# Kernel tuning notes

Measured on AMD Instinct MI355X. Metric: run time of the kernel, lower is better.

The kernel has to match this reference:

```python
import jax, jax.numpy as jnp
import numpy as np

NEG_INF = -1.0e9  # value used by masked_fill in the original

def setup_inputs() -> dict:
    key = jax.random.key(0)
    kq, kk, kv, km = jax.random.split(key, 4)
    B, H, S, D = 2, 16, 2048, 64
    query = jax.random.normal(kq, (B, H, S, D), dtype=jnp.float32)
    key_t = jax.random.normal(kk, (B, H, S, D), dtype=jnp.float32)
    value = jax.random.normal(kv, (B, H, S, D), dtype=jnp.float32)
    mask = jax.random.randint(km, (1, 1, S, S), 0, 2, dtype=jnp.int32)
    return {"query": query, "key": key_t, "value": value, "mask": mask}

def reference(query, key, value, mask):
    d_k = query.shape[-1]
    # scores: [B,H,Sq,Sk]
    scores = jnp.einsum("bhqd,bhkd->bhqk", query, key) / jnp.sqrt(jnp.float32(d_k))
    scores = jnp.where(mask == 0, jnp.float32(NEG_INF), scores)
    attn = jax.nn.softmax(scores, axis=-1)
    out = jnp.einsum("bhqk,bhkd->bhqd", attn, value)
    return (out, attn)
```

## Files before the change

kernel.cpp:

```cpp
#include <hip/hip_runtime.h>


#define S_LEN 2048
#define D_DIM 64
#define BH_N  32
#define NELEM (BH_N*S_LEN*D_DIM)

typedef __bf16 bf16;
typedef bf16 bf16x4 __attribute__((ext_vector_type(4)));
typedef bf16 bf16x8 __attribute__((ext_vector_type(8)));
typedef float f32x4 __attribute__((ext_vector_type(4)));

__device__ __attribute__((aligned(16))) bf16 g_Qb[NELEM];
__device__ __attribute__((aligned(16))) bf16 g_Kb[NELEM];
__device__ __attribute__((aligned(16))) bf16 g_VT[NELEM];
__device__ unsigned long long g_bits[S_LEN*S_LEN/64];

__device__ __forceinline__ void gload16(const bf16* g, bf16* l){
  __builtin_amdgcn_global_load_lds(
      (const __attribute__((address_space(1))) void*)g,
      (__attribute__((address_space(3))) void*)l, 16, 0, 0);
}

__global__ void cvt_qk_kernel(const float* __restrict__ Qs, const float* __restrict__ Ks){
  int i = blockIdx.x*256 + threadIdx.x;
  float4 q = reinterpret_cast<const float4*>(Qs)[i];
  float4 k = reinterpret_cast<const float4*>(Ks)[i];
  bf16x4 oq = {(bf16)q.x,(bf16)q.y,(bf16)q.z,(bf16)q.w};
  bf16x4 ok = {(bf16)k.x,(bf16)k.y,(bf16)k.z,(bf16)k.w};
  ((bf16x4*)g_Qb)[i] = oq;
  ((bf16x4*)g_Kb)[i] = ok;
}

__global__ void transpose_v_kernel(const float* __restrict__ V){
  __shared__ float sv[64][65];
  int bh = blockIdx.x >> 5;
  int k0 = (blockIdx.x & 31) << 6;
  const float* src = V + ((size_t)bh*S_LEN + k0)*D_DIM;
  #pragma unroll
  for (int i=0;i<16;i++){
    int e = threadIdx.x + i*256;
    sv[e>>6][e&63] = src[e];
  }
  __syncthreads();
  bf16* dst = g_VT + (size_t)bh*D_DIM*S_LEN + k0;
  #pragma unroll
  for (int i=0;i<16;i++){
    int e = threadIdx.x + i*256;
    int d = e>>6, k = e&63;
    dst[(size_t)d*S_LEN + k] = (bf16)sv[k][d];
  }
}

__global__ void build_bits_kernel(const int* __restrict__ mask){
  int gid = blockIdx.x*256 + threadIdx.x;
  unsigned long long b = __ballot(mask[gid] != 0);
  if ((threadIdx.x & 63) == 0) g_bits[gid >> 6] = b;
}

__global__ __launch_bounds__(256, 4)
void attn_main_kernel(float* __restrict__ out, float* __restrict__ attn){
  __shared__ __attribute__((aligned(16))) bf16 s_pool[5*64*64];
  bf16* const kd0 = s_pool;
  bf16* const kd1 = s_pool + 4096;
  bf16* const vd0 = s_pool + 8192;
  bf16* const vd1 = s_pool + 12288;
  bf16* const sp  = s_pool + 16384;

  const int tid  = threadIdx.x;
  const int wave = tid >> 6, lane = tid & 63;
  const int quad = lane >> 4, l16 = lane & 15;

  const int logical = ((blockIdx.x & 7) << 7) | (blockIdx.x >> 3);
  const int bh = logical >> 5, qb = logical & 31;
  const int q0 = qb << 6, m0 = wave << 4;

  const bf16* __restrict__ Qh  = g_Qb + ((size_t)bh*S_LEN + q0)*D_DIM;
  const bf16* __restrict__ Kh  = g_Kb + (size_t)bh*S_LEN*D_DIM;
  const bf16* __restrict__ VTh = g_VT + (size_t)bh*D_DIM*S_LEN;
  float* __restrict__ outh  = out  + ((size_t)bh*S_LEN + q0)*D_DIM;
  float* __restrict__ attnh = attn + (size_t)bh*S_LEN*S_LEN + (size_t)q0*S_LEN;

  const int s0 = tid, s1 = tid + 256;
  const int r0 = s0>>3, b0 = (s0&7)^(r0&7);
  const int r1 = s1>>3, b1 = (s1&7)^(r1&7);
  const int    gk0 = r0*D_DIM + b0*8, gk1 = r1*D_DIM + b1*8;
  const size_t gv0 = (size_t)r0*S_LEN + b0*8, gv1 = (size_t)r1*S_LEN + b1*8;
  const int lb0 = (wave<<6)*8, lb1 = (256 + (wave<<6))*8;

  gload16(Qh  + gk0, sp  + lb0);  gload16(Qh  + gk1, sp  + lb1);
  gload16(Kh  + gk0, kd0 + lb0);  gload16(Kh  + gk1, kd0 + lb1);
  gload16(VTh + gv0, vd0 + lb0);  gload16(VTh + gv1, vd0 + lb1);
  __syncthreads();

  const int arow = m0 + l16;
  const bf16x8 aq0 = *(const bf16x8*)&sp[(arow<<6) + ((quad     ^ (arow&7))<<3)];
  const bf16x8 aq1 = *(const bf16x8*)&sp[(arow<<6) + (((quad+4) ^ (arow&7))<<3)];

  float lp[4] = {0.f,0.f,0.f,0.f};
  f32x4 oacc[4];
  #pragma unroll
  for (int n=0;n<4;n++) oacc[n] = (f32x4){0.f,0.f,0.f,0.f};

  const int mrow = q0 + m0 + quad*4;
  const size_t mbase = (size_t)mrow * 32;

  for (int kt=0; kt<32; ++kt){
    bf16* const kcur = (kt&1) ? kd1 : kd0;
    bf16* const vcur = (kt&1) ? vd1 : vd0;
    if (kt < 31){
      bf16* const knxt = (kt&1) ? kd0 : kd1;
      bf16* const vnxt = (kt&1) ? vd0 : vd1;
      const bf16* Ks = Kh  + (size_t)((kt+1)<<6)*D_DIM;
      const bf16* Vs = VTh + ((kt+1)<<6);
      gload16(Ks+gk0, knxt+lb0);  gload16(Ks+gk1, knxt+lb1);
      gload16(Vs+gv0, vnxt+lb0);  gload16(Vs+gv1, vnxt+lb1);
    }
    unsigned long long wr_[4];
    #pragma unroll
    for (int r=0;r<4;r++) wr_[r] = g_bits[mbase + r*32 + kt];

    #pragma unroll
    for (int n=0;n<4;n++){
      const int krow = n*16 + l16;
      const bf16x8 bk0 = *(const bf16x8*)&kcur[(krow<<6) + ((quad     ^ (krow&7))<<3)];
      const bf16x8 bk1 = *(const bf16x8*)&kcur[(krow<<6) + (((quad+4) ^ (krow&7))<<3)];
      __builtin_amdgcn_s_setprio(1);
      f32x4 c = (f32x4){0.f,0.f,0.f,0.f};
      c = __builtin_amdgcn_mfma_f32_16x16x32_bf16(aq0, bk0, c, 0,0,0);
      c = __builtin_amdgcn_mfma_f32_16x16x32_bf16(aq1, bk1, c, 0,0,0);
      __builtin_amdgcn_s_setprio(0);
      const int shift = n*16 + l16;
      #pragma unroll
      for (int r=0;r<4;r++){
        float p = ((wr_[r] >> shift) & 1ull) ? __expf(c[r]*0.125f) : 0.f;
        lp[r] += p;
        const int prow = m0 + quad*4 + r;
        sp[(prow<<6) + (((shift>>3)^(prow&7))<<3) + (shift&7)] = (bf16)p;
      }
    }

    __builtin_amdgcn_s_setprio(1);
    #pragma unroll
    for (int s=0;s<2;s++){
      const bf16x8 pa = *(const bf16x8*)&sp[(arow<<6) + (((s*4+quad)^(arow&7))<<3)];
      #pragma unroll
      for (int n=0;n<4;n++){
        const int vrow = n*16 + l16;
        const bf16x8 vb = *(const bf16x8*)&vcur[(vrow<<6) + (((s*4+quad)^(vrow&7))<<3)];
        oacc[n] = __builtin_amdgcn_mfma_f32_16x16x32_bf16(pa, vb, oacc[n], 0,0,0);
      }
    }
    __builtin_amdgcn_s_setprio(0);
    __syncthreads();
  }

  gload16(Kh+gk0, kd0+lb0);  gload16(Kh+gk1, kd0+lb1);

  #pragma unroll
  for (int r=0;r<4;r++){
    float v = lp[r];
    #pragma unroll
    for (int off=1; off<16; off<<=1) v += __shfl_xor(v, off);
    lp[r] = 1.0f / v;
  }

  #pragma unroll
  for (int n=0;n<4;n++){
    #pragma unroll
    for (int r=0;r<4;r++)
      outh[(size_t)(m0 + quad*4 + r)*D_DIM + n*16 + l16] = oacc[n][r] * lp[r];
  }

  __syncthreads();

  for (int kt=0; kt<32; ++kt){
    bf16* const kcur = (kt&1) ? kd1 : kd0;
    if (kt < 31){
      bf16* const knxt = (kt&1) ? kd0 : kd1;
      const bf16* Ks = Kh + (size_t)((kt+1)<<6)*D_DIM;
      gload16(Ks+gk0, knxt+lb0);  gload16(Ks+gk1, knxt+lb1);
    }
    unsigned long long wr_[4];
    #pragma unroll
    for (int r=0;r<4;r++) wr_[r] = g_bits[mbase + r*32 + kt];

    #pragma unroll
    for (int n=0;n<4;n++){
      const int krow = n*16 + l16;
      const bf16x8 bk0 = *(const bf16x8*)&kcur[(krow<<6) + ((quad     ^ (krow&7))<<3)];
      const bf16x8 bk1 = *(const bf16x8*)&kcur[(krow<<6) + (((quad+4) ^ (krow&7))<<3)];
      __builtin_amdgcn_s_setprio(1);
      f32x4 c = (f32x4){0.f,0.f,0.f,0.f};
      c = __builtin_amdgcn_mfma_f32_16x16x32_bf16(aq0, bk0, c, 0,0,0);
      c = __builtin_amdgcn_mfma_f32_16x16x32_bf16(aq1, bk1, c, 0,0,0);
      __builtin_amdgcn_s_setprio(0);
      const int shift = n*16 + l16;
      #pragma unroll
      for (int r=0;r<4;r++){
        float a = ((wr_[r] >> shift) & 1ull) ? __expf(c[r]*0.125f)*lp[r] : 0.f;
        attnh[(size_t)(m0 + quad*4 + r)*S_LEN + (kt<<6) + shift] = a;
      }
    }
    __syncthreads();
  }
}

extern "C" void kernel_launch(void* const* d_in, const int* in_sizes, int n_in,
                              void* d_out, int out_size, void* d_ws, size_t ws_size,
                              hipStream_t stream){
  (void)in_sizes; (void)n_in; (void)d_ws; (void)ws_size; (void)out_size;
  const float* Q    = (const float*)d_in[0];
  const float* K    = (const float*)d_in[1];
  const float* V    = (const float*)d_in[2];
  const int*   mask = (const int*)d_in[3];
  float* out  = (float*)d_out;
  float* attn = out + (size_t)NELEM;

  cvt_qk_kernel     <<<NELEM/4/256,        256, 0, stream>>>(Q, K);
  transpose_v_kernel<<<BH_N*(S_LEN/64),    256, 0, stream>>>(V);
  build_bits_kernel <<<S_LEN*S_LEN/256,    256, 0, stream>>>(mask);
  attn_main_kernel  <<<BH_N*(S_LEN/64),    256, 0, stream>>>(out, attn);
}
```

Measured before the change: 700.0 us.

## Split key tile across wave pairs with 512-thread blocks and LDS reduction

Doubles the block to 8 waves. Each pair of waves shares a 16-row query slice and splits the 64-key tile in half, covering both the QK^T/softmax step and the PV accumulation. The partial row sums and output accumulators are combined through LDS before normalisation. The aim is more waves in flight to hide memory latency on the bandwidth-bound attention write. The cost is extra LDS traffic, an added barrier, and register pressure from the tighter launch bounds.

New measurement: 1.053 ms. 1.5x slower.

```diff
diff --git a/kernel.cpp b/kernel.cpp
--- a/kernel.cpp
+++ b/kernel.cpp
@@ -58,22 +58,26 @@
   if ((threadIdx.x & 63) == 0) g_bits[gid >> 6] = b;
 }
 
-__global__ __launch_bounds__(256, 4)
+__global__ __launch_bounds__(512, 8)
 void attn_main_kernel(float* __restrict__ out, float* __restrict__ attn){
-  __shared__ __attribute__((aligned(16))) bf16 s_pool[5*64*64];
+  __shared__ __attribute__((aligned(16))) bf16 s_pool[5*4096];
   bf16* const kd0 = s_pool;
   bf16* const kd1 = s_pool + 4096;
   bf16* const vd0 = s_pool + 8192;
   bf16* const vd1 = s_pool + 12288;
   bf16* const sp  = s_pool + 16384;
+  float* const obuf = (float*)(s_pool + 8192);
+  float* const lsum = (float*)(s_pool + 16384);
 
   const int tid  = threadIdx.x;
   const int wave = tid >> 6, lane = tid & 63;
   const int quad = lane >> 4, l16 = lane & 15;
+  const int mh = wave >> 1, kh = wave & 1;
+  const int m0 = mh << 4;
 
   const int logical = ((blockIdx.x & 7) << 7) | (blockIdx.x >> 3);
   const int bh = logical >> 5, qb = logical & 31;
-  const int q0 = qb << 6, m0 = wave << 4;
+  const int q0 = qb << 6;
 
   const bf16* __restrict__ Qh  = g_Qb + ((size_t)bh*S_LEN + q0)*D_DIM;
   const bf16* __restrict__ Kh  = g_Kb + (size_t)bh*S_LEN*D_DIM;
@@ -81,21 +85,20 @@
   float* __restrict__ outh  = out  + ((size_t)bh*S_LEN + q0)*D_DIM;
   float* __restrict__ attnh = attn + (size_t)bh*S_LEN*S_LEN + (size_t)q0*S_LEN;
 
-  const int s0 = tid, s1 = tid + 256;
-  const int r0 = s0>>3, b0 = (s0&7)^(r0&7);
-  const int r1 = s1>>3, b1 = (s1&7)^(r1&7);
-  const int    gk0 = r0*D_DIM + b0*8, gk1 = r1*D_DIM + b1*8;
-  const size_t gv0 = (size_t)r0*S_LEN + b0*8, gv1 = (size_t)r1*S_LEN + b1*8;
-  const int lb0 = (wave<<6)*8, lb1 = (256 + (wave<<6))*8;
-
-  gload16(Qh  + gk0, sp  + lb0);  gload16(Qh  + gk1, sp  + lb1);
-  gload16(Kh  + gk0, kd0 + lb0);  gload16(Kh  + gk1, kd0 + lb1);
-  gload16(VTh + gv0, vd0 + lb0);  gload16(VTh + gv1, vd0 + lb1);
+  const int r0 = tid >> 3, b0 = (tid & 7) ^ (r0 & 7);
+  const int    gk = r0*D_DIM + b0*8;
+  const size_t gv = (size_t)r0*S_LEN + b0*8;
+  const int lb = wave << 9;
+
+  gload16(Qh + gk,  sp  + lb);
+  gload16(Kh + gk,  kd0 + lb);
+  gload16(VTh + gv, vd0 + lb);
   __syncthreads();
 
   const int arow = m0 + l16;
   const bf16x8 aq0 = *(const bf16x8*)&sp[(arow<<6) + ((quad     ^ (arow&7))<<3)];
   const bf16x8 aq1 = *(const bf16x8*)&sp[(arow<<6) + (((quad+4) ^ (arow&7))<<3)];
+  __syncthreads();
 
   float lp[4] = {0.f,0.f,0.f,0.f};
   f32x4 oacc[4];
@@ -111,17 +114,16 @@
     if (kt < 31){
       bf16* const knxt = (kt&1) ? kd0 : kd1;
       bf16* const vnxt = (kt&1) ? vd0 : vd1;
-      const bf16* Ks = Kh  + (size_t)((kt+1)<<6)*D_DIM;
-      const bf16* Vs = VTh + ((kt+1)<<6);
-      gload16(Ks+gk0, knxt+lb0);  gload16(Ks+gk1, knxt+lb1);
-      gload16(Vs+gv0, vnxt+lb0);  gload16(Vs+gv1, vnxt+lb1);
+      gload16(Kh  + (size_t)((kt+1)<<6)*D_DIM + gk, knxt + lb);
+      gload16(VTh + ((kt+1)<<6) + gv,               vnxt + lb);
     }
     unsigned long long wr_[4];
     #pragma unroll
     for (int r=0;r<4;r++) wr_[r] = g_bits[mbase + r*32 + kt];
 
     #pragma unroll
-    for (int n=0;n<4;n++){
+    for (int g=0; g<2; ++g){
+      const int n = kh*2 + g;
       const int krow = n*16 + l16;
       const bf16x8 bk0 = *(const bf16x8*)&kcur[(krow<<6) + ((quad     ^ (krow&7))<<3)];
       const bf16x8 bk1 = *(const bf16x8*)&kcur[(krow<<6) + (((quad+4) ^ (krow&7))<<3)];
@@ -140,53 +142,66 @@
       }
     }
 
+    const bf16x8 pa = *(const bf16x8*)&sp[(arow<<6) + (((kh*4+quad)^(arow&7))<<3)];
     __builtin_amdgcn_s_setprio(1);
     #pragma unroll
-    for (int s=0;s<2;s++){
-      const bf16x8 pa = *(const bf16x8*)&sp[(arow<<6) + (((s*4+quad)^(arow&7))<<3)];
-      #pragma unroll
-      for (int n=0;n<4;n++){
-        const int vrow = n*16 + l16;
-        const bf16x8 vb = *(const bf16x8*)&vcur[(vrow<<6) + (((s*4+quad)^(vrow&7))<<3)];
-        oacc[n] = __builtin_amdgcn_mfma_f32_16x16x32_bf16(pa, vb, oacc[n], 0,0,0);
-      }
+    for (int n=0;n<4;n++){
+      const int vrow = n*16 + l16;
+      const bf16x8 vb = *(const bf16x8*)&vcur[(vrow<<6) + (((kh*4+quad)^(vrow&7))<<3)];
+      oacc[n] = __builtin_amdgcn_mfma_f32_16x16x32_bf16(pa, vb, oacc[n], 0,0,0);
     }
     __builtin_amdgcn_s_setprio(0);
     __syncthreads();
   }
 
-  gload16(Kh+gk0, kd0+lb0);  gload16(Kh+gk1, kd0+lb1);
+  gload16(Kh + gk, kd0 + lb);
 
   #pragma unroll
   for (int r=0;r<4;r++){
     float v = lp[r];
     #pragma unroll
     for (int off=1; off<16; off<<=1) v += __shfl_xor(v, off);
-    lp[r] = 1.0f / v;
-  }
-
-  #pragma unroll
-  for (int n=0;n<4;n++){
-    #pragma unroll
-    for (int r=0;r<4;r++)
-      outh[(size_t)(m0 + quad*4 + r)*D_DIM + n*16 + l16] = oacc[n][r] * lp[r];
-  }
-
-  __syncthreads();
+    if (l16 == 0) lsum[(kh<<6) + m0 + quad*4 + r] = v;
+  }
+  if (kh == 0){
+    #pragma unroll
+    for (int n=0;n<4;n++)
+      #pragma unroll
+      for (int r=0;r<4;r++)
+        obuf[(m0 + quad*4 + r)*64 + n*16 + l16] = oacc[n][r];
+  }
+  __syncthreads();
+
+  #pragma unroll
+  for (int r=0;r<4;r++){
+    const int row = m0 + quad*4 + r;
+    lp[r] = 1.0f / (lsum[row] + lsum[64 + row]);
+  }
+
+  if (kh == 1){
+    #pragma unroll
+    for (int n=0;n<4;n++)
+      #pragma unroll
+      for (int r=0;r<4;r++){
+        const int row = m0 + quad*4 + r;
+        outh[(size_t)row*D_DIM + n*16 + l16] =
+            (obuf[row*64 + n*16 + l16] + oacc[n][r]) * lp[r];
+      }
+  }
 
   for (int kt=0; kt<32; ++kt){
     bf16* const kcur = (kt&1) ? kd1 : kd0;
     if (kt < 31){
       bf16* const knxt = (kt&1) ? kd0 : kd1;
-      const bf16* Ks = Kh + (size_t)((kt+1)<<6)*D_DIM;
-      gload16(Ks+gk0, knxt+lb0);  gload16(Ks+gk1, knxt+lb1);
+      gload16(Kh + (size_t)((kt+1)<<6)*D_DIM + gk, knxt + lb);
     }
     unsigned long long wr_[4];
     #pragma unroll
     for (int r=0;r<4;r++) wr_[r] = g_bits[mbase + r*32 + kt];
 
     #pragma unroll
-    for (int n=0;n<4;n++){
+    for (int g=0; g<2; ++g){
+      const int n = kh*2 + g;
       const int krow = n*16 + l16;
       const bf16x8 bk0 = *(const bf16x8*)&kcur[(krow<<6) + ((quad     ^ (krow&7))<<3)];
       const bf16x8 bk1 = *(const bf16x8*)&kcur[(krow<<6) + (((quad+4) ^ (krow&7))<<3)];
@@ -220,5 +235,5 @@
   cvt_qk_kernel     <<<NELEM/4/256,        256, 0, stream>>>(Q, K);
   transpose_v_kernel<<<BH_N*(S_LEN/64),    256, 0, stream>>>(V);
   build_bits_kernel <<<S_LEN*S_LEN/256,    256, 0, stream>>>(mask);
-  attn_main_kernel  <<<BH_N*(S_LEN/64),    256, 0, stream>>>(out, attn);
-}
+  attn_main_kernel  <<<BH_N*(S_LEN/64),    512, 0, stream>>>(out, attn);
+}
```
